# Performance work log

Measured on AMD Instinct MI355X. Metric: run time of the kernel, lower is better.

## Reference

```python
import jax, jax.numpy as jnp
import numpy as np

NH, NKV, HD = 32, 8, 128      # query heads, kv heads, head dim
B, S, H = 4, 1024, 4096       # batch, per-seq tokens (prefill, no history), hidden
BLOCK = 64                    # paged KV-cache block size
BPS = S // BLOCK              # blocks per sequence


def rotate_half(x):
    x1, x2 = jnp.split(x, 2, axis=-1)
    return jnp.concatenate([-x2, x1], axis=-1)


def setup_inputs() -> dict:
    key = jax.random.key(0)
    ks = jax.random.split(key, 5)
    hidden_states = jax.random.normal(ks[0], (B * S, H), jnp.float32)
    Wq = jax.random.normal(ks[1], (H, NH * HD), jnp.float32) * 0.02
    Wk = jax.random.normal(ks[2], (H, NKV * HD), jnp.float32) * 0.02
    Wv = jax.random.normal(ks[3], (H, NKV * HD), jnp.float32) * 0.02
    Wo = jax.random.normal(ks[4], (NH * HD, H), jnp.float32) * 0.02
    # standard llama rope inverse frequencies
    inv_freq = 1.0 / (10000.0 ** (jnp.arange(0, HD, 2, dtype=jnp.float32) / HD))
    # empty paged KV cache: [num_blocks, block, n_kv_heads, head_dim]
    k_cache = jnp.zeros((B * BPS, BLOCK, NKV, HD), jnp.float32)
    v_cache = jnp.zeros((B * BPS, BLOCK, NKV, HD), jnp.float32)
    # per-token positions (prefill, history=0): 0..S-1 for each sequence
    position_ids_1d = jnp.tile(jnp.arange(S, dtype=jnp.int32), B)
    # block table: which cache block holds each logical block of each sequence
    block_offsets = jnp.arange(B * BPS, dtype=jnp.int32).reshape(B, BPS)
    return dict(hidden_states=hidden_states, Wq=Wq, Wk=Wk, Wv=Wv, Wo=Wo,
                inv_freq=inv_freq, k_cache=k_cache, v_cache=v_cache,
                position_ids_1d=position_ids_1d, block_offsets=block_offsets)


def reference(hidden_states, Wq, Wk, Wv, Wo, inv_freq, k_cache, v_cache,
              position_ids_1d, block_offsets):
    # qkv projections (contiguous-batching: tokens flattened)
    q = (hidden_states @ Wq).reshape(-1, NH, HD)
    k = (hidden_states @ Wk).reshape(-1, NKV, HD)
    v = (hidden_states @ Wv).reshape(-1, NKV, HD)

    # fused rotary: cos/sin from inv_freq at per-token 1d positions
    freqs = position_ids_1d.astype(jnp.float32)[:, None] * inv_freq[None, :]  # [T, HD/2]
    emb = jnp.concatenate([freqs, freqs], axis=-1)                            # [T, HD]
    cos = jnp.cos(emb)[:, None, :]
    sin = jnp.sin(emb)[:, None, :]
    q = q * cos + rotate_half(q) * sin
    k = k * cos + rotate_half(k) * sin

    # fill_kv_cache: scatter rotated K / raw V into paged cache via block_offsets
    flat_offsets = block_offsets.reshape(-1)
    k_blk = k.reshape(B * BPS, BLOCK, NKV, HD)
    v_blk = v.reshape(B * BPS, BLOCK, NKV, HD)
    k_cache = k_cache.at[flat_offsets].set(k_blk)
    v_cache = v_cache.at[flat_offsets].set(v_blk)

    # paged_attention_fwd: gather K/V blocks back via block table
    kk = k_cache[block_offsets].reshape(B, BPS * BLOCK, NKV, HD)  # [B, Skv, NKV, HD]
    vv = v_cache[block_offsets].reshape(B, BPS * BLOCK, NKV, HD)
    groups = NH // NKV
    kk = jnp.repeat(kk, groups, axis=2)  # repeat_kv -> [B, Skv, NH, HD]
    vv = jnp.repeat(vv, groups, axis=2)

    qb = q.reshape(B, S, NH, HD)
    scale = 1.0 / jnp.sqrt(jnp.float32(HD))
    scores = jnp.einsum('bqhd,bkhd->bhqk', qb, kk) * scale  # [B, NH, S, Skv]
    causal = jnp.arange(S)[:, None] >= jnp.arange(BPS * BLOCK)[None, :]
    scores = jnp.where(causal[None, None], scores, jnp.float32(-1e30))
    probs = jax.nn.softmax(scores, axis=-1)
    attn = jnp.einsum('bhqk,bkhd->bqhd', probs, vv).reshape(B * S, NH * HD)
    return attn @ Wo
```

## Files before the change

### kernel.cpp

```cpp
#include <hip/hip_runtime.h>
#include <cstdint>
#include <cstddef>


typedef unsigned short u16;
typedef __bf16 bf16x8 __attribute__((ext_vector_type(8)));
typedef float  f32x4  __attribute__((ext_vector_type(4)));

#define SEQ 1024
#define QKV_COLS 6144
#define NHEAD 32
#define NKVH 8
#define HDIM 128

__device__ __forceinline__ u16 f2bf(float f) {
  union { float f; uint32_t u; } v; v.f = f;
  return (u16)((v.u + 0x7fffu + ((v.u >> 16) & 1u)) >> 16);
}
__device__ __forceinline__ float bf2f(u16 x) {
  union { uint32_t u; float f; } v; v.u = ((uint32_t)x) << 16;
  return v.f;
}

typedef __attribute__((address_space(1))) const uint32_t g_u32;
typedef __attribute__((address_space(3))) uint32_t l_u32;
__device__ __forceinline__ void async_copy16(const u16* g, u16* lds_base) {
  __builtin_amdgcn_global_load_lds((g_u32*)g, (l_u32*)lds_base, 16, 0, 0);
}

__global__ void cast_f32_bf16(const float* __restrict__ in, u16* __restrict__ out, int n) {
  int i = (blockIdx.x * 256 + threadIdx.x) * 4;
  if (i >= n) return;
  float4 v = *(const float4*)&in[i];
  uint2 pk;
  pk.x = (uint32_t)f2bf(v.x) | ((uint32_t)f2bf(v.y) << 16);
  pk.y = (uint32_t)f2bf(v.z) | ((uint32_t)f2bf(v.w) << 16);
  *(uint2*)&out[i] = pk;
}

__global__ void transpose_f32_bf16(const float* __restrict__ in, u16* __restrict__ out,
                                   int R, int C) {
  __shared__ float tile[32][33];
  int c0 = blockIdx.x * 32, r0 = blockIdx.y * 32;
  int tx = threadIdx.x, ty = threadIdx.y;
  tile[ty][tx] = in[(size_t)(r0 + ty) * C + c0 + tx];
  __syncthreads();
  out[(size_t)(c0 + ty) * R + r0 + tx] = f2bf(tile[tx][ty]);
}

template <int MODE>
__global__ __launch_bounds__(256) void gemm_bt(const u16* __restrict__ A,
                                               const u16* __restrict__ Bt,
                                               void* __restrict__ Cv,
                                               u16* __restrict__ Vt,
                                               int M, int N, int K, int ldc) {
  __shared__ __align__(16) u16 As[128 * 32];
  __shared__ __align__(16) u16 Bs[128 * 32];
  const int tid = threadIdx.x;
  const int lane = tid & 63, wave = tid >> 6;
  const int l15 = lane & 15, qd = lane >> 4;
  const int wm = wave & 1, wn = wave >> 1;
  const int row0 = blockIdx.y * 128, col0 = blockIdx.x * 128;
  const int sw = (qd ^ (l15 & 3)) * 8;

  f32x4 acc[4][4] = {};
  for (int k0 = 0; k0 < K; k0 += 32) {
#pragma unroll
    for (int j = 0; j < 2; ++j) {
      const int c0 = wave * 128 + j * 64;
      const int c = c0 + lane;
      const int g = (c & ~3) | ((c & 3) ^ ((c >> 2) & 3));
      const int r = c >> 2, kc = (g & 3) * 8;
      async_copy16(&A[(size_t)(row0 + r) * K + k0 + kc], &As[c0 * 8]);
      async_copy16(&Bt[(size_t)(col0 + r) * K + k0 + kc], &Bs[c0 * 8]);
    }
    __syncthreads();
    bf16x8 af[4], bfr[4];
#pragma unroll
    for (int i = 0; i < 4; ++i) {
      af[i]  = *(const bf16x8*)&As[(wm * 64 + i * 16 + l15) * 32 + sw];
      bfr[i] = *(const bf16x8*)&Bs[(wn * 64 + i * 16 + l15) * 32 + sw];
    }
#pragma unroll
    for (int mi = 0; mi < 4; ++mi)
#pragma unroll
      for (int ni = 0; ni < 4; ++ni)
        acc[mi][ni] = __builtin_amdgcn_mfma_f32_16x16x32_bf16(af[mi], bfr[ni], acc[mi][ni], 0, 0, 0);
    __syncthreads();
  }
  if (MODE == 0 && col0 >= 5120) {
#pragma unroll
    for (int mi = 0; mi < 4; ++mi)
#pragma unroll
      for (int ni = 0; ni < 4; ++ni) {
        const int col = col0 + wn * 64 + ni * 16 + l15;
        const int dcol = col - 5120, kvh = dcol >> 7, d = dcol & 127;
        const int row = row0 + wm * 64 + mi * 16 + qd * 4;
        const int bb = row >> 10, p = row & 1023;
        ushort4 pk;
        pk.x = f2bf(acc[mi][ni][0]); pk.y = f2bf(acc[mi][ni][1]);
        pk.z = f2bf(acc[mi][ni][2]); pk.w = f2bf(acc[mi][ni][3]);
        *(ushort4*)&Vt[(((size_t)(bb * 8 + kvh) * 128) + d) * 1024 + p] = pk;
      }
    return;
  }
#pragma unroll
  for (int mi = 0; mi < 4; ++mi)
#pragma unroll
    for (int ni = 0; ni < 4; ++ni)
#pragma unroll
      for (int r = 0; r < 4; ++r) {
        int row = row0 + wm * 64 + mi * 16 + qd * 4 + r;
        int col = col0 + wn * 64 + ni * 16 + l15;
        float v = acc[mi][ni][r];
        if (MODE == 1) ((float*)Cv)[(size_t)row * ldc + col] = v;
        else           ((u16*)Cv)[(size_t)row * ldc + col] = f2bf(v);
      }
}

__global__ void rope_kernel(u16* __restrict__ qkv, const float* __restrict__ inv_freq,
                            const int* __restrict__ pos) {
  int idx = blockIdx.x * 256 + threadIdx.x;
  int t = idx / 2560;
  int r = idx - t * 2560;
  int hh = r >> 6, i = r & 63;
  float f = (float)pos[t] * inv_freq[i];
  float s, c;
  sincosf(f, &s, &c);
  size_t base = (size_t)t * QKV_COLS + hh * HDIM + i;
  float x1 = bf2f(qkv[base]), x2 = bf2f(qkv[base + 64]);
  qkv[base]      = f2bf(x1 * c - x2 * s);
  qkv[base + 64] = f2bf(x2 * c + x1 * s);
}

__global__ __launch_bounds__(512, 4) void attn_kernel(const u16* __restrict__ qkv,
                                                      const u16* __restrict__ vt,
                                                      u16* __restrict__ ao) {
  __shared__ __align__(16) u16 Ks[64 * 136];
  __shared__ __align__(16) u16 Vts[128 * 68];
  __shared__ __align__(16) u16 Ps[8][16 * 68];

  const int tid = threadIdx.x;
  const int lane = tid & 63, wave = tid >> 6;
  const int l15 = lane & 15, qd = lane >> 4;
  const int qt = blockIdx.x, h = blockIdx.y, b = blockIdx.z;
  const int q0 = qt * 128;
  const int kvh = h >> 2;
  const float scale = 0.08838834764831845f;

  bf16x8 qf[4];
  {
    const size_t qrow = (size_t)(b * SEQ + q0 + wave * 16 + l15) * QKV_COLS + h * HDIM;
#pragma unroll
    for (int s = 0; s < 4; ++s) qf[s] = *(const bf16x8*)&qkv[qrow + s * 32 + qd * 8];
  }

  f32x4 o[8] = {};
  float mrow[4] = {-__builtin_inff(), -__builtin_inff(), -__builtin_inff(), -__builtin_inff()};
  float lrow[4] = {0.f, 0.f, 0.f, 0.f};

  const int nkt = qt * 2 + 2;
  const size_t vbase0 = ((size_t)(b * NKVH + kvh) * HDIM) * SEQ;
  for (int kt = 0; kt < nkt; ++kt) {
    const int kv0 = kt * 64;
#pragma unroll
    for (int rnd = 0; rnd < 2; ++rnd) {
      int c = tid + rnd * 512;
      int kv = c >> 4, dc = (c & 15) * 8;
      *(uint4*)&Ks[kv * 136 + dc] =
          *(const uint4*)&qkv[(size_t)(b * SEQ + kv0 + kv) * QKV_COLS + 4096 + kvh * HDIM + dc];
    }
#pragma unroll
    for (int rnd = 0; rnd < 2; ++rnd) {
      int c = tid + rnd * 512;
      int d = c >> 3, kc = (c & 7) * 8;
      *(uint4*)&Vts[d * 68 + kc] = *(const uint4*)&vt[vbase0 + (size_t)d * SEQ + kv0 + kc];
    }
    __syncthreads();

    f32x4 st[4] = {};
#pragma unroll
    for (int t = 0; t < 4; ++t)
#pragma unroll
      for (int s = 0; s < 4; ++s) {
        bf16x8 kf = *(const bf16x8*)&Ks[(t * 16 + l15) * 136 + s * 32 + qd * 8];
        st[t] = __builtin_amdgcn_mfma_f32_16x16x32_bf16(qf[s], kf, st[t], 0, 0, 0);
      }

    float al[4];
#pragma unroll
    for (int r = 0; r < 4; ++r) {
      const int qpos = q0 + wave * 16 + qd * 4 + r;
      float sc[4];
#pragma unroll
      for (int t = 0; t < 4; ++t) {
        sc[t] = st[t][r] * scale;
        if (kv0 + t * 16 + l15 > qpos) sc[t] = -1e30f;
      }
      float mt = fmaxf(fmaxf(sc[0], sc[1]), fmaxf(sc[2], sc[3]));
      mt = fmaxf(mt, __shfl_xor(mt, 8));
      mt = fmaxf(mt, __shfl_xor(mt, 4));
      mt = fmaxf(mt, __shfl_xor(mt, 2));
      mt = fmaxf(mt, __shfl_xor(mt, 1));
      const float mn = fmaxf(mrow[r], mt);
      al[r] = __expf(mrow[r] - mn);
      float p[4], rs = 0.f;
#pragma unroll
      for (int t = 0; t < 4; ++t) { p[t] = __expf(sc[t] - mn); rs += p[t]; }
      rs += __shfl_xor(rs, 8);
      rs += __shfl_xor(rs, 4);
      rs += __shfl_xor(rs, 2);
      rs += __shfl_xor(rs, 1);
      lrow[r] = lrow[r] * al[r] + rs;
      mrow[r] = mn;
#pragma unroll
      for (int t = 0; t < 4; ++t)
        Ps[wave][(qd * 4 + r) * 68 + t * 16 + l15] = f2bf(p[t]);
    }
    asm volatile("s_waitcnt lgkmcnt(0)" ::: "memory");

    {
      const int srcl = (l15 >> 2) * 16;
      float a0 = __shfl(al[0], srcl), a1 = __shfl(al[1], srcl);
      float a2 = __shfl(al[2], srcl), a3 = __shfl(al[3], srcl);
      const int rr = l15 & 3;
      float aq = (rr & 2) ? ((rr & 1) ? a3 : a2) : ((rr & 1) ? a1 : a0);
#pragma unroll
      for (int dt = 0; dt < 8; ++dt) o[dt] *= aq;
    }
    {
      const bf16x8 pf0 = *(const bf16x8*)&Ps[wave][l15 * 68 + qd * 8];
      const bf16x8 pf1 = *(const bf16x8*)&Ps[wave][l15 * 68 + 32 + qd * 8];
#pragma unroll
      for (int dt = 0; dt < 8; ++dt) {
        const bf16x8 vf0 = *(const bf16x8*)&Vts[(dt * 16 + l15) * 68 + qd * 8];
        const bf16x8 vf1 = *(const bf16x8*)&Vts[(dt * 16 + l15) * 68 + 32 + qd * 8];
        o[dt] = __builtin_amdgcn_mfma_f32_16x16x32_bf16(vf0, pf0, o[dt], 0, 0, 0);
        o[dt] = __builtin_amdgcn_mfma_f32_16x16x32_bf16(vf1, pf1, o[dt], 0, 0, 0);
      }
    }
    __syncthreads();
  }

  {
    const int srcl = (l15 >> 2) * 16;
    float l0 = __shfl(lrow[0], srcl), l1 = __shfl(lrow[1], srcl);
    float l2 = __shfl(lrow[2], srcl), l3 = __shfl(lrow[3], srcl);
    const int rr = l15 & 3;
    float lq = (rr & 2) ? ((rr & 1) ? l3 : l2) : ((rr & 1) ? l1 : l0);
    const float inv = 1.0f / lq;
    const size_t obase = (size_t)(b * SEQ + q0 + wave * 16 + l15) * (NHEAD * HDIM) + h * HDIM;
#pragma unroll
    for (int dt = 0; dt < 8; ++dt) {
      ushort4 pk;
      pk.x = f2bf(o[dt][0] * inv); pk.y = f2bf(o[dt][1] * inv);
      pk.z = f2bf(o[dt][2] * inv); pk.w = f2bf(o[dt][3] * inv);
      *(ushort4*)&ao[obase + dt * 16 + qd * 4] = pk;
    }
  }
}

extern "C" void kernel_launch(void* const* d_in, const int* in_sizes, int n_in,
                              void* d_out, int out_size, void* d_ws, size_t ws_size,
                              hipStream_t stream) {
  const float* X    = (const float*)d_in[0];
  const float* Wq   = (const float*)d_in[1];
  const float* Wk   = (const float*)d_in[2];
  const float* Wv   = (const float*)d_in[3];
  const float* Wo   = (const float*)d_in[4];
  const float* invf = (const float*)d_in[5];
  const int*   pos  = (const int*)d_in[8];
  float* out = (float*)d_out;

  char* ws = (char*)d_ws;
  u16* Xbf   = (u16*)(ws + 0);
  u16* Wqkvt = (u16*)(ws + 33554432);
  u16* Wot   = (u16*)(ws + 83886080);
  u16* QKV   = (u16*)(ws + 117440512);
  u16* Vt    = (u16*)(ws + 167772160);
  u16* AO    = Xbf;

  dim3 tb32(32, 32);
  cast_f32_bf16<<<16384, 256, 0, stream>>>(X, Xbf, 16777216);
  transpose_f32_bf16<<<dim3(128, 128), tb32, 0, stream>>>(Wq, Wqkvt, 4096, 4096);
  transpose_f32_bf16<<<dim3(32, 128),  tb32, 0, stream>>>(Wk, Wqkvt + (size_t)4096 * 4096, 4096, 1024);
  transpose_f32_bf16<<<dim3(32, 128),  tb32, 0, stream>>>(Wv, Wqkvt + (size_t)5120 * 4096, 4096, 1024);
  transpose_f32_bf16<<<dim3(128, 128), tb32, 0, stream>>>(Wo, Wot, 4096, 4096);

  gemm_bt<0><<<dim3(48, 32), 256, 0, stream>>>(Xbf, Wqkvt, QKV, Vt, 4096, 6144, 4096, 6144);
  rope_kernel<<<40960, 256, 0, stream>>>(QKV, invf, pos);
  attn_kernel<<<dim3(8, 32, 4), 512, 0, stream>>>(QKV, Vt, AO);
  gemm_bt<1><<<dim3(32, 32), 256, 0, stream>>>(AO, Wot, out, Vt, 4096, 4096, 4096, 4096);
}
```

Baseline: 956.1 us.

## Rewrite GEMM with 256x256 tiles, 4-stage async pipeline and block swizzle

Replaces the single-buffered 128x128 GEMM with a 256x256-tile, 512-thread kernel that prefetches K slices three steps ahead into a four-deep LDS ring. MFMA work is split into two halves interleaved with staging of A and B, using explicit vmcnt waits, barriers and setprio. A 1D grid with an XCD-aware block swizzle replaces the 2D grid. The goal is to hide global load latency and raise data reuse per tile. The cost is more LDS (128 KB per block) and higher register pressure from the 8x4 accumulator tile. The fixed waitcnt bookkeeping is fragile.

```diff
diff --git a/kernel.cpp b/kernel.cpp
--- a/kernel.cpp
+++ b/kernel.cpp
@@ -49,53 +49,122 @@
 }
 
 template <int MODE>
-__global__ __launch_bounds__(256) void gemm_bt(const u16* __restrict__ A,
-                                               const u16* __restrict__ Bt,
-                                               void* __restrict__ Cv,
-                                               u16* __restrict__ Vt,
-                                               int M, int N, int K, int ldc) {
-  __shared__ __align__(16) u16 As[128 * 32];
-  __shared__ __align__(16) u16 Bs[128 * 32];
+__global__ __launch_bounds__(512, 2) void gemm_bt(const u16* __restrict__ A,
+                                                  const u16* __restrict__ Bt,
+                                                  void* __restrict__ Cv,
+                                                  u16* __restrict__ Vt,
+                                                  int M, int N, int K, int ldc,
+                                                  int nbx) {
+  __shared__ __align__(16) u16 smem[4][2][256 * 32];
+
   const int tid = threadIdx.x;
   const int lane = tid & 63, wave = tid >> 6;
   const int l15 = lane & 15, qd = lane >> 4;
-  const int wm = wave & 1, wn = wave >> 1;
-  const int row0 = blockIdx.y * 128, col0 = blockIdx.x * 128;
-  const int sw = (qd ^ (l15 & 3)) * 8;
-
-  f32x4 acc[4][4] = {};
-  for (int k0 = 0; k0 < K; k0 += 32) {
-#pragma unroll
-    for (int j = 0; j < 2; ++j) {
-      const int c0 = wave * 128 + j * 64;
-      const int c = c0 + lane;
-      const int g = (c & ~3) | ((c & 3) ^ ((c >> 2) & 3));
-      const int r = c >> 2, kc = (g & 3) * 8;
-      async_copy16(&A[(size_t)(row0 + r) * K + k0 + kc], &As[c0 * 8]);
-      async_copy16(&Bt[(size_t)(col0 + r) * K + k0 + kc], &Bs[c0 * 8]);
-    }
-    __syncthreads();
+  const int wm = wave >> 2, wn = wave & 3;
+
+  const int nwg = gridDim.x;
+  const int bid = (int)blockIdx.x;
+  const int swz = (bid & 7) * (nwg >> 3) + (bid >> 3);
+  const int bx = swz % nbx, by = swz / nbx;
+  const int row0 = by * 256, col0 = bx * 256;
+
+  const int sl = (qd ^ (l15 & 3) ^ (l15 >> 2)) * 8;
+
+  int soff[2], cb[2];
+#pragma unroll
+  for (int call = 0; call < 2; ++call) {
+    const int c = call * 512 + tid;
+    const int r = c >> 2, j = c & 3;
+    const int src = j ^ (r & 3) ^ ((r >> 2) & 3);
+    soff[call] = r * K + src * 8;
+    cb[call] = (call * 512 + wave * 64) * 8;
+  }
+
+  const u16* Ab = A + (size_t)row0 * K;
+  const u16* Bb = Bt + (size_t)col0 * K;
+  const int NT = K >> 5;
+
+  f32x4 acc[8][4] = {};
+
+#pragma unroll
+  for (int tt = 0; tt < 3; ++tt) {
+#pragma unroll
+    for (int call = 0; call < 2; ++call)
+      async_copy16(&Ab[tt * 32 + soff[call]], &smem[tt][0][cb[call]]);
+#pragma unroll
+    for (int call = 0; call < 2; ++call)
+      async_copy16(&Bb[tt * 32 + soff[call]], &smem[tt][1][cb[call]]);
+  }
+  asm volatile("s_waitcnt vmcnt(8)" ::: "memory");
+  __builtin_amdgcn_s_barrier();
+
+  for (int t = 0; t < NT; ++t) {
+    const int bsel = t & 3, ssel = (t + 3) & 3;
+    const u16* As = &smem[bsel][0][0];
+    const u16* Bs = &smem[bsel][1][0];
+    const bool do_stage = (t + 3) < NT;
+    const int knext = (t + 3) * 32;
+
     bf16x8 af[4], bfr[4];
 #pragma unroll
     for (int i = 0; i < 4; ++i) {
-      af[i]  = *(const bf16x8*)&As[(wm * 64 + i * 16 + l15) * 32 + sw];
-      bfr[i] = *(const bf16x8*)&Bs[(wn * 64 + i * 16 + l15) * 32 + sw];
-    }
+      af[i]  = *(const bf16x8*)&As[(wm * 128 + i * 16 + l15) * 32 + sl];
+      bfr[i] = *(const bf16x8*)&Bs[(wn * 64 + i * 16 + l15) * 32 + sl];
+    }
+    if (do_stage) {
+#pragma unroll
+      for (int call = 0; call < 2; ++call)
+        async_copy16(&Ab[knext + soff[call]], &smem[ssel][0][cb[call]]);
+    }
+    __builtin_amdgcn_s_barrier();
+    asm volatile("s_waitcnt lgkmcnt(0)" ::: "memory");
+    __builtin_amdgcn_sched_barrier(0);
+    __builtin_amdgcn_s_setprio(1);
 #pragma unroll
     for (int mi = 0; mi < 4; ++mi)
 #pragma unroll
       for (int ni = 0; ni < 4; ++ni)
         acc[mi][ni] = __builtin_amdgcn_mfma_f32_16x16x32_bf16(af[mi], bfr[ni], acc[mi][ni], 0, 0, 0);
-    __syncthreads();
-  }
+    __builtin_amdgcn_s_setprio(0);
+    __builtin_amdgcn_sched_barrier(0);
+    __builtin_amdgcn_s_barrier();
+
+#pragma unroll
+    for (int i = 0; i < 4; ++i)
+      af[i] = *(const bf16x8*)&As[(wm * 128 + (4 + i) * 16 + l15) * 32 + sl];
+    if (do_stage) {
+#pragma unroll
+      for (int call = 0; call < 2; ++call)
+        async_copy16(&Bb[knext + soff[call]], &smem[ssel][1][cb[call]]);
+    }
+    __builtin_amdgcn_s_barrier();
+    asm volatile("s_waitcnt lgkmcnt(0)" ::: "memory");
+    __builtin_amdgcn_sched_barrier(0);
+    __builtin_amdgcn_s_setprio(1);
+#pragma unroll
+    for (int mi = 0; mi < 4; ++mi)
+#pragma unroll
+      for (int ni = 0; ni < 4; ++ni)
+        acc[4 + mi][ni] = __builtin_amdgcn_mfma_f32_16x16x32_bf16(af[mi], bfr[ni], acc[4 + mi][ni], 0, 0, 0);
+    __builtin_amdgcn_s_setprio(0);
+    __builtin_amdgcn_sched_barrier(0);
+
+    if (t < NT - 1) {
+      if (t < NT - 3)       asm volatile("s_waitcnt vmcnt(8)" ::: "memory");
+      else if (t == NT - 3) asm volatile("s_waitcnt vmcnt(4)" ::: "memory");
+      else                  asm volatile("s_waitcnt vmcnt(0)" ::: "memory");
+      __builtin_amdgcn_s_barrier();
+    }
+  }
+
   if (MODE == 0 && col0 >= 5120) {
 #pragma unroll
-    for (int mi = 0; mi < 4; ++mi)
+    for (int mi = 0; mi < 8; ++mi)
 #pragma unroll
       for (int ni = 0; ni < 4; ++ni) {
         const int col = col0 + wn * 64 + ni * 16 + l15;
         const int dcol = col - 5120, kvh = dcol >> 7, d = dcol & 127;
-        const int row = row0 + wm * 64 + mi * 16 + qd * 4;
+        const int row = row0 + wm * 128 + mi * 16 + qd * 4;
         const int bb = row >> 10, p = row & 1023;
         ushort4 pk;
         pk.x = f2bf(acc[mi][ni][0]); pk.y = f2bf(acc[mi][ni][1]);
@@ -105,12 +174,12 @@
     return;
   }
 #pragma unroll
-  for (int mi = 0; mi < 4; ++mi)
+  for (int mi = 0; mi < 8; ++mi)
 #pragma unroll
     for (int ni = 0; ni < 4; ++ni)
 #pragma unroll
       for (int r = 0; r < 4; ++r) {
-        int row = row0 + wm * 64 + mi * 16 + qd * 4 + r;
+        int row = row0 + wm * 128 + mi * 16 + qd * 4 + r;
         int col = col0 + wn * 64 + ni * 16 + l15;
         float v = acc[mi][ni][r];
         if (MODE == 1) ((float*)Cv)[(size_t)row * ldc + col] = v;
@@ -287,8 +356,8 @@
   transpose_f32_bf16<<<dim3(32, 128),  tb32, 0, stream>>>(Wv, Wqkvt + (size_t)5120 * 4096, 4096, 1024);
   transpose_f32_bf16<<<dim3(128, 128), tb32, 0, stream>>>(Wo, Wot, 4096, 4096);
 
-  gemm_bt<0><<<dim3(48, 32), 256, 0, stream>>>(Xbf, Wqkvt, QKV, Vt, 4096, 6144, 4096, 6144);
+  gemm_bt<0><<<dim3(24 * 16), 512, 0, stream>>>(Xbf, Wqkvt, QKV, Vt, 4096, 6144, 4096, 6144, 24);
   rope_kernel<<<40960, 256, 0, stream>>>(QKV, invf, pos);
   attn_kernel<<<dim3(8, 32, 4), 512, 0, stream>>>(QKV, Vt, AO);
-  gemm_bt<1><<<dim3(32, 32), 256, 0, stream>>>(AO, Wot, out, Vt, 4096, 4096, 4096, 4096);
-}
+  gemm_bt<1><<<dim3(16 * 16), 512, 0, stream>>>(AO, Wot, out, Vt, 4096, 4096, 4096, 4096, 16);
+}
```

New measurement: 865.7 us. -9.5%, faster.
